# Optimization experiments

Measured on AMD Instinct MI355X. Metric: run time of the kernel, lower is better.

Reference implementation:

```python
import jax, jax.numpy as jnp
import numpy as np

NUM_HEADS = 16
D_MODEL = 1024
D_DEPTH = D_MODEL // NUM_HEADS
B, Q_LEN, M_LEN = 4, 1024, 1024
K_LEN = Q_LEN + M_LEN


def setup_inputs() -> dict:
    key = jax.random.key(0)
    ks = jax.random.split(key, 8)
    return {
        "inputs": jax.random.normal(ks[0], (B, Q_LEN, D_MODEL), jnp.float32),
        "pos_emb": jax.random.normal(ks[1], (1, K_LEN, D_MODEL), jnp.float32),
        "r_w_bias": jax.random.normal(ks[2], (NUM_HEADS, D_DEPTH), jnp.float32) * 0.01,
        "r_r_bias": jax.random.normal(ks[3], (NUM_HEADS, D_DEPTH), jnp.float32) * 0.01,
        "mems": jax.random.normal(ks[4], (B, M_LEN, D_MODEL), jnp.float32),
        "W_w": jax.random.normal(ks[5], (D_MODEL, 3 * D_MODEL), jnp.float32) * 0.01,
        "W_r": jax.random.normal(ks[6], (D_MODEL, D_MODEL), jnp.float32) * 0.01,
        "W_o": jax.random.normal(ks[7], (D_MODEL, D_MODEL), jnp.float32) * 0.01,
    }


def relative_shift(x):
    # x: [b, n, q, k] -> left-shift row i by (q - 1 - i) via pad/reshape/slice trick
    b, n, q, k = x.shape
    x = jnp.pad(x, ((0, 0), (0, 0), (0, 0), (1, 0)))
    x = x.reshape(b, n, k + 1, q)
    x = x[:, :, 1:, :]
    return x.reshape(b, n, q, k)


def relative_mask(q_len, m_len, dtype):
    # [q, m+q]: 1 at/left of current position, 0 to the right
    k = m_len + q_len
    return (jnp.arange(k)[None, :] <= (m_len + jnp.arange(q_len))[:, None]).astype(dtype)


def reference(inputs, pos_emb, r_w_bias, r_r_bias, mems, W_w, W_r, W_o):
    b, q_len, d_model = inputs.shape
    cat = jnp.concatenate([mems, inputs], axis=1)            # [b, k, d]
    k_len = cat.shape[1]
    m_len = k_len - q_len
    pe = pos_emb[:, -k_len:]                                  # [1, k, d]

    w_heads = (cat @ W_w).reshape(b, k_len, 3 * NUM_HEADS, D_DEPTH)
    w_head_q, w_head_k, w_head_v = jnp.split(w_heads, 3, axis=2)  # each [b,k,n,dd]
    w_head_q = w_head_q[:, -q_len:]                           # [b,q,n,dd]

    ac = jnp.einsum('bqnd,bknd->bnqk', w_head_q + r_w_bias, w_head_k)

    r_head_k = (pe[0] @ W_r).reshape(k_len, NUM_HEADS, D_DEPTH)
    bd = jnp.einsum('bqnd,knd->bnqk', w_head_q + r_r_bias, r_head_k)
    bd = relative_shift(bd)

    mask = relative_mask(q_len, m_len, ac.dtype)              # [q, k]
    score = (ac + bd) / jnp.asarray(D_DEPTH ** 0.5, ac.dtype)
    score = score * mask - 1e30 * (1.0 - mask)
    attn = jax.nn.softmax(score, axis=-1)

    attn_vec = jnp.einsum('bnqk,bknd->bqnd', attn, w_head_v)
    attn_vec = attn_vec.reshape(b, q_len, d_model)
    return attn_vec @ W_o
```

## Files before the change

### kernel.cpp

```cpp
#include <hip/hip_runtime.h>
#include <cstdint>
#include <cstddef>

static constexpr int QL = 1024;

typedef _Float16 half8 __attribute__((ext_vector_type(8)));
typedef _Float16 half4 __attribute__((ext_vector_type(4)));
typedef float f32x4 __attribute__((ext_vector_type(4)));

__device__ __forceinline__ const float* gemm_row_ptr(const float* A, const float* A2,
                                                     int r, int gather) {
  if (!gather) return A + (size_t)r * 1024;
  int b = r >> 11, tt = r & 2047;
  if (tt < QL) return A + ((size_t)b * QL + tt) * 1024;
  return A2 + ((size_t)b * QL + (tt - QL)) * 1024;
}

__global__ __launch_bounds__(256) void convert_a16(
    const float* __restrict__ A, const float* __restrict__ A2, int gather,
    _Float16* __restrict__ dst) {
  const int row = blockIdx.x;
  const int c = threadIdx.x * 4;
  const float* src = gemm_row_ptr(A, A2, row, gather);
  float4 v = *(const float4*)(src + c);
  half4 o = { (_Float16)v.x, (_Float16)v.y, (_Float16)v.z, (_Float16)v.w };
  *(half4*)(dst + (size_t)row * 1024 + c) = o;
}

__global__ __launch_bounds__(256) void split_w(
    const float* __restrict__ W, _Float16* __restrict__ Wt, int N) {
  __shared__ float T[64][65];
  const int nb = blockIdx.x * 64, kb = blockIdx.y * 64;
  const int t = threadIdx.x;
  {
    int row = t >> 2, c0 = (t & 3) * 16;
    const float* src = W + (size_t)(kb + row) * N + nb + c0;
#pragma unroll
    for (int c = 0; c < 16; c += 4) {
      float4 v = *(const float4*)(src + c);
      T[row][c0 + c + 0] = v.x; T[row][c0 + c + 1] = v.y;
      T[row][c0 + c + 2] = v.z; T[row][c0 + c + 3] = v.w;
    }
  }
  __syncthreads();
  {
    int nrow = t >> 2, ks = (t & 3) * 16;
    half8 hi0, hi1, lo0, lo1;
#pragma unroll
    for (int c = 0; c < 16; ++c) {
      float f = T[ks + c][nrow];
      _Float16 h = (_Float16)f;
      _Float16 l = (_Float16)(f - (float)h);
      if (c < 8) { hi0[c] = h; lo0[c] = l; } else { hi1[c - 8] = h; lo1[c - 8] = l; }
    }
    int kglob = kb + ks;
    int kt = kglob >> 5, pos = kglob & 31;
    _Float16* dst = Wt + (size_t)(nb + nrow) * 2048 + kt * 64 + pos;
    *(half8*)dst = hi0; *(half8*)(dst + 8) = hi1;
    *(half8*)(dst + 32) = lo0; *(half8*)(dst + 40) = lo1;
  }
}

__global__ __launch_bounds__(256) void gemm2(
    const _Float16* __restrict__ A16, const _Float16* __restrict__ Bt,
    int mode, const float* __restrict__ rwb,
    _Float16* __restrict__ d_q, _Float16* __restrict__ d_k,
    _Float16* __restrict__ d_v, float* __restrict__ d_f) {
  const int nbase = blockIdx.x * 128, mbase = blockIdx.y * 128;
  if (mode == 0 && nbase < 1024 && (mbase & 1024) == 0) return;

  __shared__ __align__(16) _Float16 As[128][40];
  __shared__ __align__(16) _Float16 Bs[128][72];
  const int t = threadIdx.x;
  const int lane = t & 63, w = t >> 6;
  const int ln = lane & 15, g = lane >> 4;
  const int wm = (w & 1) * 64, wn = (w >> 1) * 64;
  const int ar = t >> 1, aseg = (t & 1) * 16;
  const int br = t >> 1, bseg = (t & 1) * 32;
  const _Float16* arow = A16 + (size_t)(mbase + ar) * 1024 + aseg;
  const _Float16* brow = Bt + (size_t)(nbase + br) * 2048 + bseg;

  f32x4 acc[4][4] = {};
  for (int kt = 0; kt < 32; ++kt) {
    half8 a0 = *(const half8*)(arow + kt * 32);
    half8 a1 = *(const half8*)(arow + kt * 32 + 8);
    half8 b0 = *(const half8*)(brow + kt * 64 + 0);
    half8 b1 = *(const half8*)(brow + kt * 64 + 8);
    half8 b2 = *(const half8*)(brow + kt * 64 + 16);
    half8 b3 = *(const half8*)(brow + kt * 64 + 24);
    __syncthreads();
    *(half8*)&As[ar][aseg] = a0;      *(half8*)&As[ar][aseg + 8] = a1;
    *(half8*)&Bs[br][bseg + 0] = b0;  *(half8*)&Bs[br][bseg + 8] = b1;
    *(half8*)&Bs[br][bseg + 16] = b2; *(half8*)&Bs[br][bseg + 24] = b3;
    __syncthreads();
    half8 ah[4], bh[4], bl[4];
#pragma unroll
    for (int i = 0; i < 4; ++i)
      ah[i] = *(const half8*)&As[wm + i * 16 + ln][g * 8];
#pragma unroll
    for (int j = 0; j < 4; ++j) {
      bh[j] = *(const half8*)&Bs[wn + j * 16 + ln][g * 8];
      bl[j] = *(const half8*)&Bs[wn + j * 16 + ln][32 + g * 8];
    }
#pragma unroll
    for (int i = 0; i < 4; ++i)
#pragma unroll
      for (int j = 0; j < 4; ++j) {
        acc[i][j] = __builtin_amdgcn_mfma_f32_16x16x32_f16(ah[i], bh[j], acc[i][j], 0, 0, 0);
        acc[i][j] = __builtin_amdgcn_mfma_f32_16x16x32_f16(ah[i], bl[j], acc[i][j], 0, 0, 0);
      }
  }

  if (mode == 2) {
#pragma unroll
    for (int i = 0; i < 4; ++i)
#pragma unroll
      for (int j = 0; j < 4; ++j) {
        float* cp = d_f + (size_t)(mbase + wm + i * 16 + g * 4) * 1024 + nbase + wn + j * 16 + ln;
#pragma unroll
        for (int r = 0; r < 4; ++r) cp[(size_t)r * 1024] = acc[i][j][r];
      }
    return;
  }
  if (mode == 1) {
#pragma unroll
    for (int j = 0; j < 4; ++j) {
      int n = nbase + wn + j * 16 + ln;
      int h = n >> 6, d = n & 63;
#pragma unroll
      for (int i = 0; i < 4; ++i) {
        int m0 = mbase + wm + i * 16 + g * 4;
        _Float16* rp = d_q + ((size_t)h * 2048 + m0) * 64 + d;
#pragma unroll
        for (int r = 0; r < 4; ++r) rp[(size_t)r * 64] = (_Float16)acc[i][j][r];
      }
    }
    return;
  }
#pragma unroll
  for (int j = 0; j < 4; ++j) {
    int n = nbase + wn + j * 16 + ln;
    int sec = n >> 10;
    int c2 = n & 1023, h = c2 >> 6, d = c2 & 63;
    float bias = (sec == 0) ? rwb[c2] : 0.f;
#pragma unroll
    for (int i = 0; i < 4; ++i) {
      int m0 = mbase + wm + i * 16 + g * 4;
      int b = m0 >> 11, tt0 = m0 & 2047;
      size_t bh = (size_t)(b * 16 + h);
#pragma unroll
      for (int r = 0; r < 4; ++r) {
        int tt = tt0 + r;
        float v = acc[i][j][r];
        if (sec == 0) {
          if (tt >= 1024)
            d_q[(bh * 1024 + (tt - 1024)) * 64 + d] = (_Float16)(v + bias);
        } else if (sec == 1) {
          d_k[(bh * 2048 + tt) * 64 + d] = (_Float16)v;
        } else {
          d_v[(bh * 64 + d) * 2048 + tt] = (_Float16)v;
        }
      }
    }
  }
}

__global__ __launch_bounds__(256) void cdelta_kernel(
    const _Float16* __restrict__ r16, const float* __restrict__ rwb,
    const float* __restrict__ rrb, float* __restrict__ cd) {
  int idx = blockIdx.x * 256 + threadIdx.x;
  int jr = idx >> 4, h = idx & 15;
  const _Float16* rp = r16 + ((size_t)h * 2048 + jr) * 64;
  const float* a = rrb + h * 64;
  const float* b = rwb + h * 64;
  float s = 0.f;
#pragma unroll 8
  for (int d = 0; d < 64; ++d) s += (a[d] - b[d]) * (float)rp[d];
  cd[h * 2048 + jr] = s;
}

__global__ __launch_bounds__(256) void attn_mfma3(
    const _Float16* __restrict__ qw16, const _Float16* __restrict__ k16,
    const _Float16* __restrict__ vt16, const _Float16* __restrict__ r16,
    const float* __restrict__ cdelta, _Float16* __restrict__ av16) {
  __shared__ __align__(16) float scratch[4][80][21];
  __shared__ __align__(16) _Float16 k_s[64][72];
  __shared__ __align__(16) _Float16 vt_s[64][72];
  __shared__ __align__(16) _Float16 r_s[128][72];
  __shared__ __align__(16) _Float16 P_s[4][16][72];
  __shared__ float cdw_s[128];
  _Float16 (*qw_s)[72] = (_Float16 (*)[72])&scratch[0][0][0];

  const int id = blockIdx.x;
  const int hb = id & 63, pr = id >> 6;
  const int h = hb >> 2, b = hb & 3;
  const int bh = b * 16 + h;
  const int t = threadIdx.x;
  const int lane = t & 63, w = t >> 6;
  const int ln = lane & 15, g = lane >> 4;
  const int rb = 48 - 16 * w;

  const int s_row4 = t >> 2, s_c16 = (t & 3) * 16;
  const int s_row2 = t >> 1, s_c32 = (t & 1) * 32;

  const float* cdh = cdelta + h * 2048;
  const _Float16* kb_p = k16 + (size_t)bh * 2048 * 64;
  const _Float16* vb_p = vt16 + (size_t)bh * 64 * 2048;
  const _Float16* rb_p = r16 + (size_t)h * 2048 * 64;
  const _Float16* qb_p = qw16 + (size_t)bh * 1024 * 64;

#pragma unroll 1
  for (int phase = 0; phase < 2; ++phase) {
    const int qt = phase ? (15 - pr) : pr;
    const int qbase = qt * 64;
    const int ktiles = qt + 17;
    const int R0 = 960 - qbase;

    __syncthreads();
    {
      const _Float16* src = qb_p + (size_t)(qbase + s_row4) * 64 + s_c16;
      half8 a0 = *(const half8*)src;
      half8 a1 = *(const half8*)(src + 8);
      *(half8*)&qw_s[s_row4][s_c16] = a0;
      *(half8*)&qw_s[s_row4][s_c16 + 8] = a1;
    }
    __syncthreads();
    half8 aq0 = *(const half8*)&qw_s[16 * w + ln][g * 8];
    half8 aq1 = *(const half8*)&qw_s[16 * w + ln][32 + g * 8];
    __syncthreads();

    f32x4 O[4] = {};
    float llane[4] = {0.f, 0.f, 0.f, 0.f};

    half8 kp0, kp1, vp0, vp1, rp0, rp1, rp2, rp3;
    float cdp = 0.f;
    {
      const _Float16* kp = kb_p + (size_t)s_row4 * 64 + s_c16;
      kp0 = *(const half8*)kp; kp1 = *(const half8*)(kp + 8);
      const _Float16* vp = vb_p + (size_t)s_row4 * 2048 + s_c16;
      vp0 = *(const half8*)vp; vp1 = *(const half8*)(vp + 8);
      int rr = R0 + s_row2; rr = rr > 2047 ? 2047 : rr;
      const _Float16* rp = rb_p + (size_t)rr * 64 + s_c32;
      rp0 = *(const half8*)rp;        rp1 = *(const half8*)(rp + 8);
      rp2 = *(const half8*)(rp + 16); rp3 = *(const half8*)(rp + 24);
      if (t < 128) { int cr = R0 + t; cr = cr > 2047 ? 2047 : cr; cdp = cdh[cr]; }
    }

    for (int kt = 0; kt < ktiles; ++kt) {
      const int kbase = kt * 64;
      const int koff = (kt & 1) * 64;
      __syncthreads();
      *(half8*)&k_s[s_row4][s_c16] = kp0;  *(half8*)&k_s[s_row4][s_c16 + 8] = kp1;
      *(half8*)&vt_s[s_row4][s_c16] = vp0; *(half8*)&vt_s[s_row4][s_c16 + 8] = vp1;
      if (kt == 0) {
        *(half8*)&r_s[s_row2][s_c32] = rp0;      *(half8*)&r_s[s_row2][s_c32 + 8] = rp1;
        *(half8*)&r_s[s_row2][s_c32 + 16] = rp2; *(half8*)&r_s[s_row2][s_c32 + 24] = rp3;
        if (t < 128) cdw_s[t] = cdp;
      } else {
        const int sb = 64 - koff;
        *(half8*)&r_s[sb + s_row4][s_c16] = rp0;
        *(half8*)&r_s[sb + s_row4][s_c16 + 8] = rp1;
        if (t < 64) cdw_s[sb + t] = cdp;
      }
      __syncthreads();
      if (kt + 1 < ktiles) {
        const int kb2 = kbase + 64;
        const _Float16* kp = kb_p + (size_t)(kb2 + s_row4) * 64 + s_c16;
        kp0 = *(const half8*)kp; kp1 = *(const half8*)(kp + 8);
        const _Float16* vp = vb_p + (size_t)s_row4 * 2048 + kb2 + s_c16;
        vp0 = *(const half8*)vp; vp1 = *(const half8*)(vp + 8);
        int rr = R0 + kbase + 128 + s_row4; rr = rr > 2047 ? 2047 : rr;
        const _Float16* rp = rb_p + (size_t)rr * 64 + s_c16;
        rp0 = *(const half8*)rp; rp1 = *(const half8*)(rp + 8);
        if (t < 64) { int cr = R0 + kbase + 128 + t; cr = cr > 2047 ? 2047 : cr; cdp = cdh[cr]; }
      }

      f32x4 Sf[4];
#pragma unroll
      for (int jt = 0; jt < 4; ++jt) {
        half8 b0 = *(const half8*)&k_s[jt * 16 + ln][g * 8];
        half8 b1 = *(const half8*)&k_s[jt * 16 + ln][32 + g * 8];
        f32x4 z = {0.f, 0.f, 0.f, 0.f};
        z = __builtin_amdgcn_mfma_f32_16x16x32_f16(aq0, b0, z, 0, 0, 0);
        z = __builtin_amdgcn_mfma_f32_16x16x32_f16(aq1, b1, z, 0, 0, 0);
        Sf[jt] = z;
      }
#pragma unroll
      for (int ft = 0; ft < 5; ++ft) {
        int rrow = (rb + ft * 16 + ln + koff) & 127;
        half8 b0 = *(const half8*)&r_s[rrow][g * 8];
        half8 b1 = *(const half8*)&r_s[rrow][32 + g * 8];
        f32x4 z = {0.f, 0.f, 0.f, 0.f};
        z = __builtin_amdgcn_mfma_f32_16x16x32_f16(aq0, b0, z, 0, 0, 0);
        z = __builtin_amdgcn_mfma_f32_16x16x32_f16(aq1, b1, z, 0, 0, 0);
        float cdv = cdw_s[rrow];
        float* sc = &scratch[w][ft * 16 + ln][0];
        sc[4 * g + 0] = z[0] + cdv; sc[4 * g + 1] = z[1] + cdv;
        sc[4 * g + 2] = z[2] + cdv; sc[4 * g + 3] = z[3] + cdv;
      }
      const int climit = qbase + 16 * w + 1039 - kbase;
#pragma unroll
      for (int r = 0; r < 4; ++r) {
        float psum = 0.f;
#pragma unroll
        for (int jt = 0; jt < 4; ++jt) {
          int cw = jt * 16 + ln + 15 - 4 * g - r;
          float tv = scratch[w][cw][4 * g + r];
          float x = (Sf[jt][r] + tv) * 0.125f;
          float p = (cw > climit) ? 0.f : __expf(x);
          psum += p;
          P_s[w][4 * g + r][jt * 16 + ln] = (_Float16)p;
        }
        llane[r] += psum;
      }
      half8 pA0 = *(const half8*)&P_s[w][ln][g * 8];
      half8 pA1 = *(const half8*)&P_s[w][ln][32 + g * 8];
#pragma unroll
      for (int dt = 0; dt < 4; ++dt) {
        half8 b0 = *(const half8*)&vt_s[dt * 16 + ln][g * 8];
        half8 b1 = *(const half8*)&vt_s[dt * 16 + ln][32 + g * 8];
        O[dt] = __builtin_amdgcn_mfma_f32_16x16x32_f16(pA0, b0, O[dt], 0, 0, 0);
        O[dt] = __builtin_amdgcn_mfma_f32_16x16x32_f16(pA1, b1, O[dt], 0, 0, 0);
      }
    }

#pragma unroll
    for (int r = 0; r < 4; ++r) {
      float ls = llane[r];
      ls += __shfl_xor(ls, 1, 64);
      ls += __shfl_xor(ls, 2, 64);
      ls += __shfl_xor(ls, 4, 64);
      ls += __shfl_xor(ls, 8, 64);
      float inv = 1.f / ls;
      int qrow = qbase + 16 * w + 4 * g + r;
      _Float16* op = av16 + ((size_t)b * 1024 + qrow) * 1024 + h * 64 + ln;
#pragma unroll
      for (int dt = 0; dt < 4; ++dt) op[dt * 16] = (_Float16)(O[dt][r] * inv);
    }
  }
}

extern "C" void kernel_launch(void* const* d_in, const int* in_sizes, int n_in,
                              void* d_out, int out_size, void* d_ws, size_t ws_size,
                              hipStream_t stream) {
  const float* inputs  = (const float*)d_in[0];
  const float* pos_emb = (const float*)d_in[1];
  const float* rwb     = (const float*)d_in[2];
  const float* rrb     = (const float*)d_in[3];
  const float* mems    = (const float*)d_in[4];
  const float* W_w     = (const float*)d_in[5];
  const float* W_r     = (const float*)d_in[6];
  const float* W_o     = (const float*)d_in[7];
  float* out = (float*)d_out;

  _Float16* hws = (_Float16*)d_ws;
  _Float16* a16   = hws;
  _Float16* pe16  = a16  + (size_t)8192 * 1024;
  _Float16* qw16  = pe16 + (size_t)2048 * 1024;
  _Float16* k16   = qw16 + (size_t)64 * 1024 * 64;
  _Float16* vt16  = k16  + (size_t)64 * 2048 * 64;
  _Float16* r16   = vt16 + (size_t)64 * 64 * 2048;
  _Float16* av16  = r16  + (size_t)16 * 2048 * 64;
  _Float16* wwt   = av16 + (size_t)4096 * 1024;
  _Float16* wrt   = wwt  + (size_t)3072 * 2048;
  _Float16* wot   = wrt  + (size_t)1024 * 2048;
  float*    cdelta = (float*)(wot + (size_t)1024 * 2048);

  convert_a16<<<8192, 256, 0, stream>>>(mems, inputs, 1, a16);
  convert_a16<<<2048, 256, 0, stream>>>(pos_emb, nullptr, 0, pe16);
  split_w<<<dim3(48, 16), 256, 0, stream>>>(W_w, wwt, 3072);
  split_w<<<dim3(16, 16), 256, 0, stream>>>(W_r, wrt, 1024);
  split_w<<<dim3(16, 16), 256, 0, stream>>>(W_o, wot, 1024);
  gemm2<<<dim3(24, 64), 256, 0, stream>>>(a16, wwt, 0, rwb, qw16, k16, vt16, nullptr);
  gemm2<<<dim3(8, 16), 256, 0, stream>>>(pe16, wrt, 1, rwb, r16, nullptr, nullptr, nullptr);
  cdelta_kernel<<<128, 256, 0, stream>>>(r16, rwb, rrb, cdelta);
  attn_mfma3<<<512, 256, 0, stream>>>(qw16, k16, vt16, r16, cdelta, av16);
  gemm2<<<dim3(8, 32), 256, 0, stream>>>(av16, wot, 2, rwb, nullptr, nullptr, nullptr, out);
}
```

Before: 441.5 us.

## Drop low-half weight correction for projection GEMMs and prefetch tiles into registers

```diff
diff --git a/kernel.cpp b/kernel.cpp
--- a/kernel.cpp
+++ b/kernel.cpp
@@ -76,38 +76,49 @@
   const int ln = lane & 15, g = lane >> 4;
   const int wm = (w & 1) * 64, wn = (w >> 1) * 64;
   const int ar = t >> 1, aseg = (t & 1) * 16;
-  const int br = t >> 1, bseg = (t & 1) * 32;
+  const int br = t >> 1;
+  const int bseg = (mode == 2) ? (t & 1) * 32 : (t & 1) * 16;
   const _Float16* arow = A16 + (size_t)(mbase + ar) * 1024 + aseg;
   const _Float16* brow = Bt + (size_t)(nbase + br) * 2048 + bseg;
 
+  half8 pa0, pa1, pb0, pb1, pb2, pb3;
+  pa0 = *(const half8*)(arow);      pa1 = *(const half8*)(arow + 8);
+  pb0 = *(const half8*)(brow);      pb1 = *(const half8*)(brow + 8);
+  if (mode == 2) { pb2 = *(const half8*)(brow + 16); pb3 = *(const half8*)(brow + 24); }
+
   f32x4 acc[4][4] = {};
   for (int kt = 0; kt < 32; ++kt) {
-    half8 a0 = *(const half8*)(arow + kt * 32);
-    half8 a1 = *(const half8*)(arow + kt * 32 + 8);
-    half8 b0 = *(const half8*)(brow + kt * 64 + 0);
-    half8 b1 = *(const half8*)(brow + kt * 64 + 8);
-    half8 b2 = *(const half8*)(brow + kt * 64 + 16);
-    half8 b3 = *(const half8*)(brow + kt * 64 + 24);
-    __syncthreads();
-    *(half8*)&As[ar][aseg] = a0;      *(half8*)&As[ar][aseg + 8] = a1;
-    *(half8*)&Bs[br][bseg + 0] = b0;  *(half8*)&Bs[br][bseg + 8] = b1;
-    *(half8*)&Bs[br][bseg + 16] = b2; *(half8*)&Bs[br][bseg + 24] = b3;
-    __syncthreads();
+    __syncthreads();
+    *(half8*)&As[ar][aseg] = pa0;     *(half8*)&As[ar][aseg + 8] = pa1;
+    *(half8*)&Bs[br][bseg] = pb0;     *(half8*)&Bs[br][bseg + 8] = pb1;
+    if (mode == 2) { *(half8*)&Bs[br][bseg + 16] = pb2; *(half8*)&Bs[br][bseg + 24] = pb3; }
+    __syncthreads();
+    if (kt + 1 < 32) {
+      const _Float16* ap = arow + (kt + 1) * 32;
+      const _Float16* bp = brow + (kt + 1) * 64;
+      pa0 = *(const half8*)(ap);      pa1 = *(const half8*)(ap + 8);
+      pb0 = *(const half8*)(bp);      pb1 = *(const half8*)(bp + 8);
+      if (mode == 2) { pb2 = *(const half8*)(bp + 16); pb3 = *(const half8*)(bp + 24); }
+    }
     half8 ah[4], bh[4], bl[4];
 #pragma unroll
     for (int i = 0; i < 4; ++i)
       ah[i] = *(const half8*)&As[wm + i * 16 + ln][g * 8];
 #pragma unroll
-    for (int j = 0; j < 4; ++j) {
+    for (int j = 0; j < 4; ++j)
       bh[j] = *(const half8*)&Bs[wn + j * 16 + ln][g * 8];
-      bl[j] = *(const half8*)&Bs[wn + j * 16 + ln][32 + g * 8];
+    if (mode == 2) {
+#pragma unroll
+      for (int j = 0; j < 4; ++j)
+        bl[j] = *(const half8*)&Bs[wn + j * 16 + ln][32 + g * 8];
     }
 #pragma unroll
     for (int i = 0; i < 4; ++i)
 #pragma unroll
       for (int j = 0; j < 4; ++j) {
         acc[i][j] = __builtin_amdgcn_mfma_f32_16x16x32_f16(ah[i], bh[j], acc[i][j], 0, 0, 0);
-        acc[i][j] = __builtin_amdgcn_mfma_f32_16x16x32_f16(ah[i], bl[j], acc[i][j], 0, 0, 0);
+        if (mode == 2)
+          acc[i][j] = __builtin_amdgcn_mfma_f32_16x16x32_f16(ah[i], bl[j], acc[i][j], 0, 0, 0);
       }
   }
 
```

After: 382.8 us. -13.3%, faster.
